# Optimization experiments

Hardware: AMD Instinct MI355X
Metric: run time of the kernel (lower is better)

## Reference

```python
import jax, jax.numpy as jnp
import numpy as np

N = 50000       # nodes
E = 400000      # edges (avg degree 8)
IN, HID, OUT, ED = 128, 256, 128, 64
EXP = 2          # GENConv MLP expansion
EPS_MSG = 1e-7   # GENConv eps added to relu(msg)
EPS_BN = 1e-5    # BatchNorm eps
EPS_SM = 1e-16   # PyG softmax denominator eps


def _lin(key, fi, fo):
    w = jax.random.normal(key, (fi, fo), jnp.float32) / np.float32(np.sqrt(fi))
    return w, jnp.zeros((fo,), jnp.float32)


def _layer_params(key, fi, fo, ed):
    ks = jax.random.split(key, 5)
    Wsrc, bsrc = _lin(ks[0], fi, fo)
    Wdst, bdst = _lin(ks[1], fi, fo)
    We, be = _lin(ks[2], ed, fo)
    W1, b1 = _lin(ks[3], fo, fo * EXP)
    W2, b2 = _lin(ks[4], fo * EXP, fo)
    g = jnp.ones((fo * EXP,), jnp.float32)   # BN gamma
    bt = jnp.zeros((fo * EXP,), jnp.float32) # BN beta
    return dict(Wsrc=Wsrc, bsrc=bsrc, Wdst=Wdst, bdst=bdst, We=We, be=be,
                W1=W1, b1=b1, g=g, bt=bt, W2=W2, b2=b2)


def setup_inputs() -> dict:
    key = jax.random.key(0)
    k0, k1, k2, k3, k4 = jax.random.split(key, 5)
    inp = {
        'x': jax.random.normal(k0, (N, IN), jnp.float32),
        'edge_index': jax.random.randint(k1, (2, E), 0, N, jnp.int32),
        'edge_attr': jax.random.normal(k2, (E, ED), jnp.float32),
    }
    for pref, p in (('l1_', _layer_params(k3, IN, HID, ED)),
                    ('l2_', _layer_params(k4, HID, OUT, ED))):
        for n, v in p.items():
            inp[pref + n] = v
    return inp


def _genconv(x, src, dst, ea, Wsrc, bsrc, Wdst, bdst, We, be, W1, b1, g, bt, W2, b2):
    n = x.shape[0]
    h = x @ Wsrc + bsrc                          # [N, F] lin_src
    e = ea @ We + be                             # [E, F] lin_edge
    msg = jax.nn.relu(h[src] + e) + EPS_MSG      # [E, F] message
    # softmax aggregation over destination nodes (t = 1.0)
    mx = jax.ops.segment_max(msg, dst, num_segments=n)
    ex = jnp.exp(msg - mx[dst])
    den = jax.ops.segment_sum(ex, dst, num_segments=n)
    alpha = ex / (den[dst] + EPS_SM)
    agg = jax.ops.segment_sum(alpha * msg, dst, num_segments=n)  # [N, F]
    out = agg + (x @ Wdst + bdst)                # residual lin_dst
    # MLP: Linear -> BatchNorm(train stats) -> ReLU -> Linear
    h1 = out @ W1 + b1                           # [N, 2F]
    mu = h1.mean(0)
    var = h1.var(0)
    h1 = (h1 - mu) * jax.lax.rsqrt(var + EPS_BN) * g + bt
    return jax.nn.relu(h1) @ W2 + b2


def reference(x, edge_index, edge_attr,
              l1_Wsrc, l1_bsrc, l1_Wdst, l1_bdst, l1_We, l1_be,
              l1_W1, l1_b1, l1_g, l1_bt, l1_W2, l1_b2,
              l2_Wsrc, l2_bsrc, l2_Wdst, l2_bdst, l2_We, l2_be,
              l2_W1, l2_b1, l2_g, l2_bt, l2_W2, l2_b2):
    src, dst = edge_index[0], edge_index[1]
    h = _genconv(x, src, dst, edge_attr,
                 l1_Wsrc, l1_bsrc, l1_Wdst, l1_bdst, l1_We, l1_be,
                 l1_W1, l1_b1, l1_g, l1_bt, l1_W2, l1_b2)
    h = jax.nn.relu(h)
    return _genconv(h, src, dst, edge_attr,
                    l2_Wsrc, l2_bsrc, l2_Wdst, l2_bdst, l2_We, l2_be,
                    l2_W1, l2_b1, l2_g, l2_bt, l2_W2, l2_b2)
```

## Files before the change

### kernel.cpp

```cpp
#include <hip/hip_runtime.h>

typedef unsigned short u16;
typedef unsigned int u32;
typedef __attribute__((ext_vector_type(8))) short sv8;
typedef __attribute__((ext_vector_type(4))) float fv4;
typedef __attribute__((ext_vector_type(4))) unsigned short us4;
typedef __attribute__((ext_vector_type(2))) unsigned short us2;

__device__ __forceinline__ u16 f2b(float x) {
    union { float f; u32 u; } a; a.f = x;
    u32 r = a.u + 0x7FFFu + ((a.u >> 16) & 1u);
    return (u16)(r >> 16);
}
__device__ __forceinline__ float b2f(u16 h) {
    union { u32 u; float f; } a; a.u = ((u32)h) << 16;
    return a.f;
}

__device__ __forceinline__ void gll16(const void* g, void* l) {
    __builtin_amdgcn_global_load_lds((__attribute__((address_space(1))) void*)g,
                                     (__attribute__((address_space(3))) void*)l,
                                     16, 0, 0);
}

template<bool AF32, bool AAFF, int EPI, bool STATS>
__global__ __launch_bounds__(256) void k_gemm(
    const void* __restrict__ Aptr, const u16* __restrict__ Wt,
    const float* __restrict__ bias, void* __restrict__ Cptr,
    int M, int K, int F,
    const float* __restrict__ sc, const float* __restrict__ sh,
    float* __restrict__ sums, float* __restrict__ sumsq)
{
    __shared__ u16 As[64][68];
    __shared__ u16 Bs[64][68];
    __shared__ u16 Cs[64][68];
    const int t = threadIdx.x, w = t >> 6, l = t & 63;
    const int n0 = blockIdx.x * 64, m0 = blockIdx.y * 64;
    const int arow = t >> 2;
    const size_t gr = (size_t)(m0 + arow < M ? m0 + arow : M - 1);

    fv4 acc[4] = {};

    for (int k0 = 0; k0 < K; k0 += 64) {
        #pragma unroll
        for (int i = 0; i < 2; ++i) {
            const int acol = (((t & 3) << 1) + i) << 3;
            const int kb = k0 + acol;
            sv8 av;
            if constexpr (AF32) {
                const float* Af = (const float*)Aptr;
                fv4 u0 = *(const fv4*)(Af + gr * K + kb);
                fv4 u1 = *(const fv4*)(Af + gr * K + kb + 4);
                #pragma unroll
                for (int j = 0; j < 4; ++j) { av[j] = (short)f2b(u0[j]); av[j + 4] = (short)f2b(u1[j]); }
            } else if constexpr (AAFF) {
                sv8 v = *(const sv8*)((const u16*)Aptr + gr * K + kb);
                fv4 c0 = *(const fv4*)(sc + kb), c1 = *(const fv4*)(sc + kb + 4);
                fv4 d0 = *(const fv4*)(sh + kb), d1 = *(const fv4*)(sh + kb + 4);
                #pragma unroll
                for (int j = 0; j < 4; ++j) {
                    av[j]     = (short)f2b(fmaxf(b2f((u16)v[j])     * c0[j] + d0[j], 0.f));
                    av[j + 4] = (short)f2b(fmaxf(b2f((u16)v[j + 4]) * c1[j] + d1[j], 0.f));
                }
            } else {
                av = *(const sv8*)((const u16*)Aptr + gr * K + kb);
            }
            *(sv8*)&As[arow][acol] = av;
            *(sv8*)&Bs[arow][acol] = *(const sv8*)(Wt + (size_t)(n0 + arow) * K + kb);
        }
        __syncthreads();

        #pragma unroll
        for (int kk = 0; kk < 2; ++kk) {
            sv8 a = *(const sv8*)&As[(w << 4) + (l & 15)][((kk << 2) + (l >> 4)) << 3];
            #pragma unroll
            for (int ct = 0; ct < 4; ++ct) {
                sv8 b = *(const sv8*)&Bs[(ct << 4) + (l & 15)][((kk << 2) + (l >> 4)) << 3];
                acc[ct] = __builtin_amdgcn_mfma_f32_16x16x32_bf16(a, b, acc[ct], 0, 0, 0);
            }
        }
        __syncthreads();
    }

    const int lr0 = (w << 4) + ((l >> 4) << 2);
    #pragma unroll
    for (int ct = 0; ct < 4; ++ct) {
        const int col = (ct << 4) + (l & 15);
        const float bv = bias[n0 + col];
        float s = 0.f, s2 = 0.f;
        #pragma unroll
        for (int r = 0; r < 4; ++r) {
            const int lrow = lr0 + r;
            const bool valid = (m0 + lrow) < M;
            float v = acc[ct][r] + bv;
            if constexpr (STATS) { if (valid) { s += v; s2 += v * v; } }
            if constexpr (EPI == 1) v = fmaxf(v, 0.f);
            if constexpr (EPI == 3) {
                if (valid) ((float*)Cptr)[(size_t)(m0 + lrow) * F + n0 + col] = v;
            } else {
                Cs[lrow][col] = f2b(v);
            }
        }
        if constexpr (STATS) {
            s  += __shfl_xor(s, 16);  s  += __shfl_xor(s, 32);
            s2 += __shfl_xor(s2, 16); s2 += __shfl_xor(s2, 32);
            if (l < 16) { unsafeAtomicAdd(&sums[n0 + col], s); unsafeAtomicAdd(&sumsq[n0 + col], s2); }
        }
    }
    if constexpr (EPI != 3) {
        __syncthreads();
        const int lrow = t >> 2, c0 = (t & 3) << 4;
        if (m0 + lrow < M) {
            u16* Cb = (u16*)Cptr + (size_t)(m0 + lrow) * F + n0 + c0;
            *(sv8*)Cb       = *(const sv8*)&Cs[lrow][c0];
            *(sv8*)(Cb + 8) = *(const sv8*)&Cs[lrow][c0 + 8];
        }
    }
}

template<int FN>
__global__ __launch_bounds__(256) void k_egemm3(
    const float* __restrict__ ea, const int* __restrict__ perm,
    const u16* __restrict__ Wt, const float* __restrict__ bias,
    u16* __restrict__ Cbuf)
{
    __shared__ u16 Bs[FN * 64];
    const int t = threadIdx.x, w = t >> 6, l = t & 63;
    const int m0 = blockIdx.x * 64;

    constexpr int BISS = FN / 32;
    #pragma unroll
    for (int i = 0; i < BISS; ++i) {
        int slot = ((w * BISS + i) << 6) + l;
        int row = slot >> 3, g = (slot & 7) ^ (row & 7);
        gll16(Wt + (size_t)row * 64 + g * 8, Bs + ((w * BISS + i) << 6) * 8);
    }

    const int g0 = l >> 4;
    const int gr = m0 + (w << 4) + (l & 15);
    const int prow = perm[gr];
    const float* ar = ea + (size_t)prow * 64 + (g0 << 3);
    fv4 u0 = *(const fv4*)ar;
    fv4 u1 = *(const fv4*)(ar + 4);
    fv4 u2 = *(const fv4*)(ar + 32);
    fv4 u3 = *(const fv4*)(ar + 36);
    sv8 a0, a1;
    #pragma unroll
    for (int j = 0; j < 4; ++j) {
        a0[j] = (short)f2b(u0[j]); a0[j + 4] = (short)f2b(u1[j]);
        a1[j] = (short)f2b(u2[j]); a1[j + 4] = (short)f2b(u3[j]);
    }
    __syncthreads();

    fv4 acc[FN / 16];
    #pragma unroll
    for (int ct = 0; ct < FN / 16; ++ct) {
        int Brow = (ct << 4) + (l & 15);
        sv8 b0 = *(const sv8*)&Bs[(Brow * 8 + ((g0)     ^ (Brow & 7))) * 8];
        sv8 b1 = *(const sv8*)&Bs[(Brow * 8 + ((g0 + 4) ^ (Brow & 7))) * 8];
        fv4 z = {};
        z = __builtin_amdgcn_mfma_f32_16x16x32_bf16(a0, b0, z, 0, 0, 0);
        acc[ct] = __builtin_amdgcn_mfma_f32_16x16x32_bf16(a1, b1, z, 0, 0, 0);
    }

    const int r0 = (w << 4) + ((l >> 4) << 2);
    #pragma unroll
    for (int ct = 0; ct < FN / 16; ++ct) {
        const int col = (ct << 4) + (l & 15);
        const float bv = bias[col];
        #pragma unroll
        for (int r = 0; r < 4; ++r) {
            const int row = m0 + r0 + r;
            u32 my = (u32)f2b(acc[ct][r] + bv);
            u32 ot = (u32)__shfl_xor((int)my, 1);
            if (!(l & 1))
                *(u32*)(Cbuf + (size_t)row * FN + col) = (my & 0xFFFFu) | (ot << 16);
        }
    }
}

__global__ void k_hist(const int* __restrict__ dst, int* __restrict__ counts, int E) {
    int i = blockIdx.x * 256 + threadIdx.x;
    if (i < E) atomicAdd(&counts[dst[i]], 1);
}

__global__ __launch_bounds__(256) void k_psum(const int* __restrict__ counts,
                                              int* __restrict__ bsum, int n) {
    int i = blockIdx.x * 256 + threadIdx.x;
    int v = (i < n) ? counts[i] : 0;
    #pragma unroll
    for (int o = 1; o < 64; o <<= 1) v += __shfl_xor(v, o);
    __shared__ int ws[4];
    if ((threadIdx.x & 63) == 0) ws[threadIdx.x >> 6] = v;
    __syncthreads();
    if (threadIdx.x == 0) bsum[blockIdx.x] = ws[0] + ws[1] + ws[2] + ws[3];
}

__global__ __launch_bounds__(256) void k_bscan(const int* __restrict__ bsum,
                                               int* __restrict__ boff, int nb) {
    __shared__ int sm[256];
    int t = threadIdx.x;
    int v = (t < nb) ? bsum[t] : 0;
    sm[t] = v; __syncthreads();
    #pragma unroll
    for (int o = 1; o < 256; o <<= 1) {
        int u = (t >= o) ? sm[t - o] : 0;
        __syncthreads();
        sm[t] += u;
        __syncthreads();
    }
    if (t < nb) boff[t] = sm[t] - v;
}

__global__ __launch_bounds__(256) void k_windp(const int* __restrict__ counts,
                                               const int* __restrict__ boff,
                                               int* __restrict__ indptr,
                                               int* __restrict__ cursors, int n) {
    __shared__ int sm[256];
    const int t = threadIdx.x, i = blockIdx.x * 256 + t;
    int v = (i < n) ? counts[i] : 0;
    sm[t] = v; __syncthreads();
    #pragma unroll
    for (int o = 1; o < 256; o <<= 1) {
        int u = (t >= o) ? sm[t - o] : 0;
        __syncthreads();
        sm[t] += u;
        __syncthreads();
    }
    int excl = sm[t] - v + boff[blockIdx.x];
    if (i < n) { indptr[i] = excl; cursors[i] = excl; }
    if (i == n - 1) indptr[n] = excl + v;
}

__global__ void k_scatter(const int* __restrict__ dst, const int* __restrict__ src,
                          int* __restrict__ cursors, int* __restrict__ perm,
                          int* __restrict__ srcp, int E) {
    int i = blockIdx.x * 256 + threadIdx.x;
    if (i < E) {
        int p = atomicAdd(&cursors[dst[i]], 1);
        perm[p] = i;
        srcp[p] = src[i];
    }
}

template<int F, int VPT>
__global__ __launch_bounds__(256) void k_agg(
    const u16* __restrict__ e, const u16* __restrict__ hhd,
    const int* __restrict__ srcp, const int* __restrict__ indptr,
    u16* __restrict__ out, int N)
{
    const int nid = blockIdx.x * 4 + (threadIdx.x >> 6);
    if (nid >= N) return;
    const int c0 = (threadIdx.x & 63) * VPT;
    const int S = 2 * F;
    const int p0 = indptr[nid], p1 = indptr[nid + 1];
    float den[VPT] = {}, num[VPT] = {};

    auto LOADP = [&](int p, u16* ev, u16* hv) {
        const int s = srcp[p];
        if constexpr (VPT == 4) {
            *(us4*)ev = *(const us4*)&e[(size_t)p * F + c0];
            *(us4*)hv = *(const us4*)&hhd[(size_t)s * S + c0];
        } else {
            *(us2*)ev = *(const us2*)&e[(size_t)p * F + c0];
            *(us2*)hv = *(const us2*)&hhd[(size_t)s * S + c0];
        }
    };
    auto ACCUM = [&](const u16* ev, const u16* hv) {
        #pragma unroll
        for (int j = 0; j < VPT; ++j) {
            float x = fmaxf(b2f(ev[j]) + b2f(hv[j]), 0.f) + 1e-7f;
            float ex = __expf(x);
            den[j] += ex;
            num[j] += ex * x;
        }
    };

    if (p0 < p1) {
        u16 ev[VPT], hv[VPT];
        LOADP(p0, ev, hv);
        for (int p = p0 + 1; p < p1; ++p) {
            u16 ev2[VPT], hv2[VPT];
            LOADP(p, ev2, hv2);
            ACCUM(ev, hv);
            #pragma unroll
            for (int j = 0; j < VPT; ++j) { ev[j] = ev2[j]; hv[j] = hv2[j]; }
        }
        ACCUM(ev, hv);
    }

    #pragma unroll
    for (int j = 0; j < VPT; ++j) {
        float o = num[j] / (den[j] + 1e-16f) + b2f(hhd[(size_t)nid * S + F + c0 + j]);
        out[(size_t)nid * F + c0 + j] = f2b(o);
    }
}

struct WtDesc { const float* W; u16* D; int K; int F; int end; };
struct WtPack { WtDesc d[10]; };

__global__ void k_wtall(WtPack p, int total) {
    int i = blockIdx.x * 256 + threadIdx.x;
    if (i >= total) return;
    int s = 0, base = 0;
    while (i >= p.d[s].end) { base = p.d[s].end; ++s; }
    int loc = i - base;
    int K = p.d[s].K, F = p.d[s].F;
    int f = loc / K, k = loc - f * K;
    p.d[s].D[loc] = f2b(p.d[s].W[(size_t)k * F + f]);
}

__global__ void k_bcat(const float* __restrict__ bsrc1, const float* __restrict__ bdst1,
                       const float* __restrict__ bsrc2, const float* __restrict__ bdst2,
                       float* __restrict__ bcat1, float* __restrict__ bcat2) {
    int t = threadIdx.x;
    bcat1[t] = bsrc1[t];
    bcat1[256 + t] = bdst1[t];
    if (t < 128) {
        bcat2[t] = bsrc2[t];
        bcat2[128 + t] = bdst2[t];
    }
}

__global__ void k_bnfinal(const float* __restrict__ sums, const float* __restrict__ sumsq,
                          const float* __restrict__ g, const float* __restrict__ bt,
                          float* __restrict__ scale, float* __restrict__ shift,
                          int C, float invN)
{
    int c = blockIdx.x * 256 + threadIdx.x;
    if (c < C) {
        float mu  = sums[c] * invN;
        float var = sumsq[c] * invN - mu * mu;
        float s   = g[c] * rsqrtf(var + 1e-5f);
        scale[c] = s;
        shift[c] = bt[c] - mu * s;
    }
}

extern "C" void kernel_launch(void* const* d_in, const int* in_sizes, int n_in,
                              void* d_out, int out_size, void* d_ws, size_t ws_size,
                              hipStream_t stream)
{
    const int IN = 128, HID = 256, OUT = 128, ED = 64;
    const int N = in_sizes[0] / IN;
    const int E = in_sizes[1] / 2;

    const float* x   = (const float*)d_in[0];
    const int*   src = (const int*)d_in[1];
    const int*   dst = src + E;
    const float* ea  = (const float*)d_in[2];
    auto F32 = [&](int i) { return (const float*)d_in[i]; };
    const float *Wsrc1 = F32(3),  *bsrc1 = F32(4),  *Wdst1 = F32(5),  *bdst1 = F32(6),
                *We1   = F32(7),  *be1   = F32(8),  *W11   = F32(9),  *b11   = F32(10),
                *g1    = F32(11), *bt1   = F32(12), *W21   = F32(13), *b21   = F32(14);
    const float *Wsrc2 = F32(15), *bsrc2 = F32(16), *Wdst2 = F32(17), *bdst2 = F32(18),
                *We2   = F32(19), *be2   = F32(20), *W12   = F32(21), *b12   = F32(22),
                *g2    = F32(23), *bt2   = F32(24), *W22   = F32(25), *b22   = F32(26);

    char* wp = (char*)d_ws;
    auto carve = [&](size_t bytes) -> void* {
        void* r = (void*)wp; wp += (bytes + 255) & ~(size_t)255; return r;
    };
    u16* wcat1  = (u16*)carve((size_t)HID * IN * 2);
    u16* wdst1t = (u16*)carve((size_t)HID * IN * 2);
    u16* we1t   = (u16*)carve((size_t)HID * ED * 2);
    u16* w11t   = (u16*)carve((size_t)(2 * HID) * HID * 2);
    u16* w21t   = (u16*)carve((size_t)HID * (2 * HID) * 2);
    u16* wcat2  = (u16*)carve((size_t)OUT * HID * 2);
    u16* wdst2t = (u16*)carve((size_t)OUT * HID * 2);
    u16* we2t   = (u16*)carve((size_t)OUT * ED * 2);
    u16* w12t   = (u16*)carve((size_t)(2 * OUT) * OUT * 2);
    u16* w22t   = (u16*)carve((size_t)OUT * (2 * OUT) * 2);
    int* counts  = (int*)carve((size_t)N * 4);
    int* indptr  = (int*)carve((size_t)(N + 1) * 4);
    int* cursors = (int*)carve((size_t)N * 4);
    int* perm    = (int*)carve((size_t)E * 4);
    int* srcp    = (int*)carve((size_t)E * 4);
    int* bsum    = (int*)carve((size_t)256 * 4);
    int* boff    = (int*)carve((size_t)256 * 4);
    u16* hhd  = (u16*)carve((size_t)N * 512 * 2);
    u16* x2   = (u16*)carve((size_t)N * HID * 2);
    u16* ebuf = (u16*)carve((size_t)E * HID * 2);
    float* stats1 = (float*)carve((size_t)1024 * 4);
    float* stats2 = (float*)carve((size_t)512 * 4);
    float* ss1    = (float*)carve((size_t)1024 * 4);
    float* ss2    = (float*)carve((size_t)512 * 4);
    float* bcat1  = (float*)carve((size_t)512 * 4);
    float* bcat2  = (float*)carve((size_t)256 * 4);
    u16* h1 = ebuf;

    hipMemsetAsync(counts, 0, (size_t)N * 4, stream);
    hipMemsetAsync(stats1, 0, (size_t)(1024 + 512) * 4, stream);
    k_hist<<<dim3((E + 255) / 256), dim3(256), 0, stream>>>(dst, counts, E);
    const int nb = (N + 255) / 256;
    k_psum<<<dim3(nb), dim3(256), 0, stream>>>(counts, bsum, N);
    k_bscan<<<dim3(1), dim3(256), 0, stream>>>(bsum, boff, nb);
    k_windp<<<dim3(nb), dim3(256), 0, stream>>>(counts, boff, indptr, cursors, N);
    k_scatter<<<dim3((E + 255) / 256), dim3(256), 0, stream>>>(dst, src, cursors, perm, srcp, E);

    WtPack wpk; int acc_end = 0;
    auto addw = [&](int idx, const float* W, u16* D, int K, int F) {
        acc_end += K * F;
        wpk.d[idx] = WtDesc{W, D, K, F, acc_end};
    };
    addw(0, Wsrc1, wcat1,  IN, HID);   addw(1, Wdst1, wdst1t, IN, HID);
    addw(2, We1,   we1t,   ED, HID);   addw(3, W11,   w11t,   HID, 2 * HID);
    addw(4, W21,   w21t,   2 * HID, HID);
    addw(5, Wsrc2, wcat2,  HID, OUT);  addw(6, Wdst2, wdst2t, HID, OUT);
    addw(7, We2,   we2t,   ED, OUT);   addw(8, W12,   w12t,   OUT, 2 * OUT);
    addw(9, W22,   w22t,   2 * OUT, OUT);
    k_wtall<<<dim3((acc_end + 255) / 256), dim3(256), 0, stream>>>(wpk, acc_end);
    k_bcat<<<dim3(1), dim3(256), 0, stream>>>(bsrc1, bdst1, bsrc2, bdst2, bcat1, bcat2);

    const int gm = (N + 63) / 64;

    k_gemm<true, false, 0, false><<<dim3(8, gm), dim3(256), 0, stream>>>(
        x, wcat1, bcat1, hhd, N, IN, 512, nullptr, nullptr, nullptr, nullptr);
    k_egemm3<256><<<dim3(E / 64), dim3(256), 0, stream>>>(ea, perm, we1t, be1, ebuf);
    k_agg<256, 4><<<dim3((N + 3) / 4), dim3(256), 0, stream>>>(ebuf, hhd, srcp, indptr, x2, N);
    k_gemm<false, false, 0, true><<<dim3(8, gm), dim3(256), 0, stream>>>(
        x2, w11t, b11, h1, N, HID, 512, nullptr, nullptr, stats1, stats1 + 512);
    k_bnfinal<<<dim3(2), dim3(256), 0, stream>>>(
        stats1, stats1 + 512, g1, bt1, ss1, ss1 + 512, 512, 1.f / N);
    k_gemm<false, true, 1, false><<<dim3(4, gm), dim3(256), 0, stream>>>(
        h1, w21t, b21, x2, N, 512, HID, ss1, ss1 + 512, nullptr, nullptr);

    k_gemm<false, false, 0, false><<<dim3(4, gm), dim3(256), 0, stream>>>(
        x2, wcat2, bcat2, hhd, N, HID, 256, nullptr, nullptr, nullptr, nullptr);
    k_egemm3<128><<<dim3(E / 64), dim3(256), 0, stream>>>(ea, perm, we2t, be2, ebuf);
    k_agg<128, 2><<<dim3((N + 3) / 4), dim3(256), 0, stream>>>(ebuf, hhd, srcp, indptr, x2, N);
    k_gemm<false, false, 0, true><<<dim3(4, gm), dim3(256), 0, stream>>>(
        x2, w12t, b12, h1, N, OUT, 256, nullptr, nullptr, stats2, stats2 + 256);
    k_bnfinal<<<dim3(1), dim3(256), 0, stream>>>(
        stats2, stats2 + 256, g2, bt2, ss2, ss2 + 256, 256, 1.f / N);
    k_gemm<false, true, 3, false><<<dim3(2, gm), dim3(256), 0, stream>>>(
        h1, w22t, b22, d_out, N, HID, OUT, ss2, ss2 + 256, nullptr, nullptr);
}
```

Measured before the change: 701.0 us.

## Fuse edge-feature GEMM into softmax aggregation, per-node wave MFMA over edges

Merges the edge linear projection into the aggregation kernel. Each wave now handles one destination node and runs MFMA on 16-edge chunks of pre-permuted bf16 edge attributes, then applies relu, exp and the weighted sums in registers. A new k_permea kernel converts and permutes edge_attr to bf16 once, and both layers reuse it. This removes the E×F bf16 edge buffer write and read per layer. In exchange, low-degree nodes waste MFMA lanes, and the hhd gathers are now scalar per element rather than vectorised.

```diff
diff --git a/kernel.cpp b/kernel.cpp
--- a/kernel.cpp
+++ b/kernel.cpp
@@ -5,7 +5,6 @@
 typedef __attribute__((ext_vector_type(8))) short sv8;
 typedef __attribute__((ext_vector_type(4))) float fv4;
 typedef __attribute__((ext_vector_type(4))) unsigned short us4;
-typedef __attribute__((ext_vector_type(2))) unsigned short us2;
 
 __device__ __forceinline__ u16 f2b(float x) {
     union { float f; u32 u; } a; a.f = x;
@@ -118,15 +117,16 @@
     }
 }
 
-template<int FN>
-__global__ __launch_bounds__(256) void k_egemm3(
-    const float* __restrict__ ea, const int* __restrict__ perm,
-    const u16* __restrict__ Wt, const float* __restrict__ bias,
-    u16* __restrict__ Cbuf)
+template<int FN, int S>
+__global__ __launch_bounds__(256) void k_eagg3(
+    const u16* __restrict__ eab, const u16* __restrict__ Wt,
+    const float* __restrict__ bias, const u16* __restrict__ hhd,
+    const int* __restrict__ srcp, const int* __restrict__ indptr,
+    u16* __restrict__ out, int N)
 {
     __shared__ u16 Bs[FN * 64];
     const int t = threadIdx.x, w = t >> 6, l = t & 63;
-    const int m0 = blockIdx.x * 64;
+    const int g0 = l >> 4, le = l & 15;
 
     constexpr int BISS = FN / 32;
     #pragma unroll
@@ -135,48 +135,85 @@
         int row = slot >> 3, g = (slot & 7) ^ (row & 7);
         gll16(Wt + (size_t)row * 64 + g * 8, Bs + ((w * BISS + i) << 6) * 8);
     }
-
-    const int g0 = l >> 4;
-    const int gr = m0 + (w << 4) + (l & 15);
-    const int prow = perm[gr];
-    const float* ar = ea + (size_t)prow * 64 + (g0 << 3);
-    fv4 u0 = *(const fv4*)ar;
-    fv4 u1 = *(const fv4*)(ar + 4);
-    fv4 u2 = *(const fv4*)(ar + 32);
-    fv4 u3 = *(const fv4*)(ar + 36);
-    sv8 a0, a1;
-    #pragma unroll
-    for (int j = 0; j < 4; ++j) {
-        a0[j] = (short)f2b(u0[j]); a0[j + 4] = (short)f2b(u1[j]);
-        a1[j] = (short)f2b(u2[j]); a1[j + 4] = (short)f2b(u3[j]);
-    }
     __syncthreads();
 
-    fv4 acc[FN / 16];
-    #pragma unroll
-    for (int ct = 0; ct < FN / 16; ++ct) {
-        int Brow = (ct << 4) + (l & 15);
-        sv8 b0 = *(const sv8*)&Bs[(Brow * 8 + ((g0)     ^ (Brow & 7))) * 8];
-        sv8 b1 = *(const sv8*)&Bs[(Brow * 8 + ((g0 + 4) ^ (Brow & 7))) * 8];
-        fv4 z = {};
-        z = __builtin_amdgcn_mfma_f32_16x16x32_bf16(a0, b0, z, 0, 0, 0);
-        acc[ct] = __builtin_amdgcn_mfma_f32_16x16x32_bf16(a1, b1, z, 0, 0, 0);
-    }
-
-    const int r0 = (w << 4) + ((l >> 4) << 2);
-    #pragma unroll
-    for (int ct = 0; ct < FN / 16; ++ct) {
-        const int col = (ct << 4) + (l & 15);
-        const float bv = bias[col];
+    const int nid = blockIdx.x * 4 + w;
+    if (nid >= N) return;
+    const int p0 = indptr[nid], p1 = indptr[nid + 1];
+
+    float den[FN / 16] = {}, num[FN / 16] = {};
+    float bv[FN / 16];
+    #pragma unroll
+    for (int ct = 0; ct < FN / 16; ++ct) bv[ct] = bias[(ct << 4) + le];
+
+    for (int cb = p0; cb < p1; cb += 16) {
+        int p = cb + le; if (p > p1 - 1) p = p1 - 1;
+        const u16* er = eab + (size_t)p * 64;
+        sv8 a0 = *(const sv8*)(er + (g0 << 3));
+        sv8 a1 = *(const sv8*)(er + 32 + (g0 << 3));
+
+        int s4[4];
         #pragma unroll
         for (int r = 0; r < 4; ++r) {
-            const int row = m0 + r0 + r;
-            u32 my = (u32)f2b(acc[ct][r] + bv);
-            u32 ot = (u32)__shfl_xor((int)my, 1);
-            if (!(l & 1))
-                *(u32*)(Cbuf + (size_t)row * FN + col) = (my & 0xFFFFu) | (ot << 16);
-        }
-    }
+            int pe = cb + (g0 << 2) + r;
+            s4[r] = (pe < p1) ? srcp[pe] : -1;
+        }
+
+        #pragma unroll
+        for (int ct = 0; ct < FN / 16; ++ct) {
+            const int Brow = (ct << 4) + le;
+            sv8 b0 = *(const sv8*)&Bs[(Brow * 8 + ((g0)     ^ (Brow & 7))) * 8];
+            sv8 b1 = *(const sv8*)&Bs[(Brow * 8 + ((g0 + 4) ^ (Brow & 7))) * 8];
+            fv4 z = {};
+            z = __builtin_amdgcn_mfma_f32_16x16x32_bf16(a0, b0, z, 0, 0, 0);
+            fv4 acc = __builtin_amdgcn_mfma_f32_16x16x32_bf16(a1, b1, z, 0, 0, 0);
+            #pragma unroll
+            for (int r = 0; r < 4; ++r) {
+                if (s4[r] >= 0) {
+                    float hv = b2f(hhd[(size_t)s4[r] * S + (ct << 4) + le]);
+                    float x = fmaxf(acc[r] + bv[ct] + hv, 0.f) + 1e-7f;
+                    float e = __expf(x);
+                    den[ct] += e;
+                    num[ct] += e * x;
+                }
+            }
+        }
+    }
+
+    #pragma unroll
+    for (int ct = 0; ct < FN / 16; ++ct) {
+        den[ct] += __shfl_xor(den[ct], 16); den[ct] += __shfl_xor(den[ct], 32);
+        num[ct] += __shfl_xor(num[ct], 16); num[ct] += __shfl_xor(num[ct], 32);
+    }
+
+    const u16* hd = hhd + (size_t)nid * S + FN;
+    #pragma unroll
+    for (int ct = 0; ct < FN / 16; ++ct) {
+        if ((ct & 3) == g0) {
+            const int col = (ct << 4) + le;
+            float o = num[ct] / (den[ct] + 1e-16f) + b2f(hd[col]);
+            out[(size_t)nid * FN + col] = f2b(o);
+        }
+    }
+}
+
+__global__ __launch_bounds__(256) void k_permea(
+    const float* __restrict__ ea, const int* __restrict__ perm,
+    u16* __restrict__ eab)
+{
+    const int t = threadIdx.x;
+    const int p = blockIdx.x * 64 + (t >> 2);
+    const int q = t & 3;
+    const float* srcr = ea + (size_t)perm[p] * 64 + q * 16;
+    u16 o[16];
+    #pragma unroll
+    for (int i = 0; i < 4; ++i) {
+        fv4 u = *(const fv4*)(srcr + i * 4);
+        o[i * 4 + 0] = f2b(u[0]); o[i * 4 + 1] = f2b(u[1]);
+        o[i * 4 + 2] = f2b(u[2]); o[i * 4 + 3] = f2b(u[3]);
+    }
+    *(sv8*)(eab + (size_t)p * 64 + q * 16)     = *(sv8*)&o[0];
+    *(sv8*)(eab + (size_t)p * 64 + q * 16 + 8) = *(sv8*)&o[8];
 }
 
 __global__ void k_hist(const int* __restrict__ dst, int* __restrict__ counts, int E) {
@@ -240,59 +277,6 @@
         int p = atomicAdd(&cursors[dst[i]], 1);
         perm[p] = i;
         srcp[p] = src[i];
-    }
-}
-
-template<int F, int VPT>
-__global__ __launch_bounds__(256) void k_agg(
-    const u16* __restrict__ e, const u16* __restrict__ hhd,
-    const int* __restrict__ srcp, const int* __restrict__ indptr,
-    u16* __restrict__ out, int N)
-{
-    const int nid = blockIdx.x * 4 + (threadIdx.x >> 6);
-    if (nid >= N) return;
-    const int c0 = (threadIdx.x & 63) * VPT;
-    const int S = 2 * F;
-    const int p0 = indptr[nid], p1 = indptr[nid + 1];
-    float den[VPT] = {}, num[VPT] = {};
-
-    auto LOADP = [&](int p, u16* ev, u16* hv) {
-        const int s = srcp[p];
-        if constexpr (VPT == 4) {
-            *(us4*)ev = *(const us4*)&e[(size_t)p * F + c0];
-            *(us4*)hv = *(const us4*)&hhd[(size_t)s * S + c0];
-        } else {
-            *(us2*)ev = *(const us2*)&e[(size_t)p * F + c0];
-            *(us2*)hv = *(const us2*)&hhd[(size_t)s * S + c0];
-        }
-    };
-    auto ACCUM = [&](const u16* ev, const u16* hv) {
-        #pragma unroll
-        for (int j = 0; j < VPT; ++j) {
-            float x = fmaxf(b2f(ev[j]) + b2f(hv[j]), 0.f) + 1e-7f;
-            float ex = __expf(x);
-            den[j] += ex;
-            num[j] += ex * x;
-        }
-    };
-
-    if (p0 < p1) {
-        u16 ev[VPT], hv[VPT];
-        LOADP(p0, ev, hv);
-        for (int p = p0 + 1; p < p1; ++p) {
-            u16 ev2[VPT], hv2[VPT];
-            LOADP(p, ev2, hv2);
-            ACCUM(ev, hv);
-            #pragma unroll
-            for (int j = 0; j < VPT; ++j) { ev[j] = ev2[j]; hv[j] = hv2[j]; }
-        }
-        ACCUM(ev, hv);
-    }
-
-    #pragma unroll
-    for (int j = 0; j < VPT; ++j) {
-        float o = num[j] / (den[j] + 1e-16f) + b2f(hhd[(size_t)nid * S + F + c0 + j]);
-        out[(size_t)nid * F + c0 + j] = f2b(o);
     }
 }
 
@@ -378,16 +362,16 @@
     int* srcp    = (int*)carve((size_t)E * 4);
     int* bsum    = (int*)carve((size_t)256 * 4);
     int* boff    = (int*)carve((size_t)256 * 4);
+    u16* eab  = (u16*)carve((size_t)E * ED * 2);
     u16* hhd  = (u16*)carve((size_t)N * 512 * 2);
     u16* x2   = (u16*)carve((size_t)N * HID * 2);
-    u16* ebuf = (u16*)carve((size_t)E * HID * 2);
+    u16* h1   = (u16*)carve((size_t)N * (2 * HID) * 2);
     float* stats1 = (float*)carve((size_t)1024 * 4);
     float* stats2 = (float*)carve((size_t)512 * 4);
     float* ss1    = (float*)carve((size_t)1024 * 4);
     float* ss2    = (float*)carve((size_t)512 * 4);
     float* bcat1  = (float*)carve((size_t)512 * 4);
     float* bcat2  = (float*)carve((size_t)256 * 4);
-    u16* h1 = ebuf;
 
     hipMemsetAsync(counts, 0, (size_t)N * 4, stream);
     hipMemsetAsync(stats1, 0, (size_t)(1024 + 512) * 4, stream);
@@ -397,6 +381,7 @@
     k_bscan<<<dim3(1), dim3(256), 0, stream>>>(bsum, boff, nb);
     k_windp<<<dim3(nb), dim3(256), 0, stream>>>(counts, boff, indptr, cursors, N);
     k_scatter<<<dim3((E + 255) / 256), dim3(256), 0, stream>>>(dst, src, cursors, perm, srcp, E);
+    k_permea<<<dim3(E / 64), dim3(256), 0, stream>>>(ea, perm, eab);
 
     WtPack wpk; int acc_end = 0;
     auto addw = [&](int idx, const float* W, u16* D, int K, int F) {
@@ -413,11 +398,12 @@
     k_bcat<<<dim3(1), dim3(256), 0, stream>>>(bsrc1, bdst1, bsrc2, bdst2, bcat1, bcat2);
 
     const int gm = (N + 63) / 64;
+    const int ga = (N + 3) / 4;
 
     k_gemm<true, false, 0, false><<<dim3(8, gm), dim3(256), 0, stream>>>(
         x, wcat1, bcat1, hhd, N, IN, 512, nullptr, nullptr, nullptr, nullptr);
-    k_egemm3<256><<<dim3(E / 64), dim3(256), 0, stream>>>(ea, perm, we1t, be1, ebuf);
-    k_agg<256, 4><<<dim3((N + 3) / 4), dim3(256), 0, stream>>>(ebuf, hhd, srcp, indptr, x2, N);
+    k_eagg3<256, 512><<<dim3(ga), dim3(256), 0, stream>>>(
+        eab, we1t, be1, hhd, srcp, indptr, x2, N);
     k_gemm<false, false, 0, true><<<dim3(8, gm), dim3(256), 0, stream>>>(
         x2, w11t, b11, h1, N, HID, 512, nullptr, nullptr, stats1, stats1 + 512);
     k_bnfinal<<<dim3(2), dim3(256), 0, stream>>>(
@@ -427,8 +413,8 @@
 
     k_gemm<false, false, 0, false><<<dim3(4, gm), dim3(256), 0, stream>>>(
         x2, wcat2, bcat2, hhd, N, HID, 256, nullptr, nullptr, nullptr, nullptr);
-    k_egemm3<128><<<dim3(E / 64), dim3(256), 0, stream>>>(ea, perm, we2t, be2, ebuf);
-    k_agg<128, 2><<<dim3((N + 3) / 4), dim3(256), 0, stream>>>(ebuf, hhd, srcp, indptr, x2, N);
+    k_eagg3<128, 256><<<dim3(ga), dim3(256), 0, stream>>>(
+        eab, we2t, be2, hhd, srcp, indptr, x2, N);
     k_gemm<false, false, 0, true><<<dim3(4, gm), dim3(256), 0, stream>>>(
         x2, w12t, b12, h1, N, OUT, 256, nullptr, nullptr, stats2, stats2 + 256);
     k_bnfinal<<<dim3(1), dim3(256), 0, stream>>>(
```

Result: slower. 1.161 ms (+65.6%).
